# Optimization experiments

Hardware: AMD Instinct MI355X
Metric: run time of the kernel (lower is better)

The kernel has to match this reference:

```python
import jax, jax.numpy as jnp
import numpy as np

B, T, E, H = 64, 512, 256, 128


def setup_inputs() -> dict:
    key = jax.random.key(0)
    ks = jax.random.split(key, 7)
    s = 1.0 / np.sqrt(H)  # PyTorch LSTM default init range
    inputs = jax.random.normal(ks[0], (B, T, E), jnp.float32)
    labels = jax.random.randint(ks[1], (B, T), 0, H)
    W_ih = jax.random.uniform(ks[2], (4 * H, E), jnp.float32, -s, s)
    W_hh = jax.random.uniform(ks[3], (4 * H, H), jnp.float32, -s, s)
    b_ih = jax.random.uniform(ks[4], (4 * H,), jnp.float32, -s, s)
    b_hh = jax.random.uniform(ks[5], (4 * H,), jnp.float32, -s, s)
    transition = jax.random.uniform(ks[6], (H, H), jnp.float32)  # torch.rand
    return {"inputs": inputs, "labels": labels, "W_ih": W_ih, "W_hh": W_hh,
            "b_ih": b_ih, "b_hh": b_hh, "transition": transition}


def _lstm(x, W_ih, W_hh, b_ih, b_hh):
    # x: (T, B, E) -> hs: (T, B, H). PyTorch gate order: i, f, g, o.
    Bn = x.shape[1]
    Hn = W_hh.shape[1]

    def step(carry, xt):
        h, c = carry
        g = xt @ W_ih.T + b_ih + h @ W_hh.T + b_hh  # (B, 4H)
        i, f, gg, o = jnp.split(g, 4, axis=-1)
        c = jax.nn.sigmoid(f) * c + jax.nn.sigmoid(i) * jnp.tanh(gg)
        h = jax.nn.sigmoid(o) * jnp.tanh(c)
        return (h, c), h

    h0 = jnp.zeros((Bn, Hn), x.dtype)
    (_, _), hs = jax.lax.scan(step, (h0, h0), x)
    return hs


def reference(inputs, labels, W_ih, W_hh, b_ih, b_hh, transition):
    x = inputs.transpose(1, 0, 2)  # (T, B, E)
    trans = jax.nn.softmax(transition, axis=1)  # row-softmax transition
    hs = _lstm(x, W_ih, W_hh, b_ih, b_hh)  # (T, B, H)
    Hbth = jax.nn.softmax(hs, axis=2).transpose(1, 0, 2)  # (B, T, H)

    # gold-path score Pr: emissions at gold tags + transition scores
    emit = jnp.take_along_axis(Hbth, labels[:, :, None], axis=2)[..., 0].sum(axis=1)  # (B,)
    tr_score = trans[labels[:, :-1], labels[:, 1:]].sum(axis=1)  # (B,)
    Pr = emit + tr_score

    # CRF forward algorithm (partition score Ps) via scan over time
    pre0 = Hbth[:, 0, :] + trans[0]  # (B, H)

    def crf_step(pre, h_t):
        # Z[b, i, j] = pre[b, i] + trans[i, j] + h_t[b, j]
        Z = pre[:, :, None] + trans[None] + h_t[:, None, :]
        return jax.nn.logsumexp(Z, axis=1), None

    pre, _ = jax.lax.scan(crf_step, pre0, Hbth[:, 1:, :].transpose(1, 0, 2))
    Ps = jax.nn.logsumexp(pre + trans[-1][None, :], axis=1)  # (B,)

    return (Ps - Pr).sum()
```

## Files before the change

kernel.cpp:

```cpp
#include <hip/hip_runtime.h>
#include <hip/hip_bf16.h>
#include <cstdint>

#define BB 64
#define TT 512
#define EE 256
#define HH 128
#define G4 512

typedef _Float16 half2_t __attribute__((ext_vector_type(2)));
typedef _Float16 f16x4 __attribute__((ext_vector_type(4)));
typedef _Float16 f16x8 __attribute__((ext_vector_type(8)));
typedef float f32x4 __attribute__((ext_vector_type(4)));

#define BC(x) __builtin_bit_cast(half2_t, x)

#define BAR() asm volatile("s_waitcnt lgkmcnt(0)\n\ts_barrier" ::: "memory")

__device__ __forceinline__ float fdot2f(half2_t a, half2_t b, float c) {
#if defined(__has_builtin)
#if __has_builtin(__builtin_amdgcn_fdot2)
  return __builtin_amdgcn_fdot2(a, b, c, false);
#else
  return c + (float)a[0] * (float)b[0] + (float)a[1] * (float)b[1];
#endif
#else
  return c + (float)a[0] * (float)b[0] + (float)a[1] * (float)b[1];
#endif
}

__device__ __forceinline__ float rcp_(float x) { return __builtin_amdgcn_rcpf(x); }
__device__ __forceinline__ float tanh_(float x) {
  float ax = fabsf(x);
  float e = __expf(-2.f * ax);
  float r = (1.f - e) * rcp_(1.f + e);
  return copysignf(r, x);
}

__device__ __forceinline__ float readlane_f(float x, int lane) {
#if defined(__has_builtin)
#if __has_builtin(__builtin_amdgcn_readlane)
  return __builtin_bit_cast(float, __builtin_amdgcn_readlane(__builtin_bit_cast(int, x), lane));
#else
  return __shfl(x, lane);
#endif
#else
  return __shfl(x, lane);
#endif
}

#if defined(__has_builtin)
#if __has_builtin(__builtin_amdgcn_update_dpp)
#define HAVE_DPP 1
#endif
#endif

#ifdef HAVE_DPP
#define DPP_SHL(dst, src, N)                                                   \
  dst = __builtin_bit_cast(float, __builtin_amdgcn_update_dpp(                 \
            0, __builtin_bit_cast(int, src), 0x100 | (N), 0xf, 0xf, true))
#define DPP_QSWAP(dst, src)                                                    \
  dst = __builtin_bit_cast(float, __builtin_amdgcn_update_dpp(                 \
            0, __builtin_bit_cast(int, src), 0xB1, 0xf, 0xf, true))
#else
#define DPP_SHL(dst, src, N) dst = __shfl((src), (threadIdx.x & 63) + (N))
#define DPP_QSWAP(dst, src) dst = __shfl_xor((src), 1)
#endif

__device__ __forceinline__ float wave_sum64_bcast(float x) {
#ifdef HAVE_DPP
#define DPP_ADD(ctrl)                                                          \
  {                                                                            \
    int _t = __builtin_amdgcn_update_dpp(0, __builtin_bit_cast(int, x), ctrl,  \
                                         0xf, 0xf, true);                      \
    x += __builtin_bit_cast(float, _t);                                        \
  }
  DPP_ADD(0x111)
  DPP_ADD(0x112)
  DPP_ADD(0x114)
  DPP_ADD(0x118)
  DPP_ADD(0x142)
  DPP_ADD(0x143)
#undef DPP_ADD
  return readlane_f(x, 63);
#else
#pragma unroll
  for (int s = 1; s <= 32; s <<= 1) x += __shfl_xor(x, s);
  return x;
#endif
}

__device__ __host__ __forceinline__ int permj(int j) {
  return ((j & 127) << 2) | (j >> 7);
}

__global__ __launch_bounds__(128) void prep_kernel(
    const float* __restrict__ transition, const float* __restrict__ W_ih,
    float* __restrict__ trans, _Float16* __restrict__ W16) {
  const int bid = blockIdx.x, t = threadIdx.x;
  if (bid < 128) {
    __shared__ float red[2];
    float v = transition[bid * HH + t];
    float m = v;
#pragma unroll
    for (int s = 32; s >= 1; s >>= 1) m = fmaxf(m, __shfl_xor(m, s));
    if ((t & 63) == 0) red[t >> 6] = m;
    __syncthreads();
    m = fmaxf(red[0], red[1]);
    float e = __expf(v - m);
    float s = e;
#pragma unroll
    for (int k = 32; k >= 1; k >>= 1) s += __shfl_xor(s, k);
    __syncthreads();
    if ((t & 63) == 0) red[t >> 6] = s;
    __syncthreads();
    trans[bid * HH + t] = e * rcp_(red[0] + red[1]);
  } else {
    const int base = (bid - 128) * 1024 + t * 8;
    const int row = base >> 8;
    const int col = base & 255;
    float4 v0 = *(const float4*)(W_ih + base);
    float4 v1 = *(const float4*)(W_ih + base + 4);
    f16x8 h;
    h[0] = (_Float16)v0.x; h[1] = (_Float16)v0.y;
    h[2] = (_Float16)v0.z; h[3] = (_Float16)v0.w;
    h[4] = (_Float16)v1.x; h[5] = (_Float16)v1.y;
    h[6] = (_Float16)v1.z; h[7] = (_Float16)v1.w;
    *(f16x8*)(W16 + (size_t)permj(row) * EE + col) = h;
  }
}

__global__ __launch_bounds__(256) void gemm_in(
    const float* __restrict__ A, const _Float16* __restrict__ W16,
    const float* __restrict__ b_ih, const float* __restrict__ b_hh,
    float* __restrict__ out) {
  __shared__ _Float16 As[64][264];
  const int t = threadIdx.x;
  const int m0 = blockIdx.x * 64;
  const int n0 = blockIdx.y * 256;
  {
    const int c4 = t & 63, r0 = t >> 6;
#pragma unroll
    for (int p = 0; p < 16; ++p) {
      const int row = r0 + 4 * p;
      float4 v = *(const float4*)(A + (size_t)(m0 + row) * EE + c4 * 4);
      f16x4 h;
      h[0] = (_Float16)v.x; h[1] = (_Float16)v.y;
      h[2] = (_Float16)v.z; h[3] = (_Float16)v.w;
      *(f16x4*)&As[row][c4 * 4] = h;
    }
  }
  __syncthreads();
  const int w = t >> 6, L = t & 63;
  const int lrow = L & 15, quad = L >> 4, lk = quad * 8;
  f32x4 acc[4][4] = {};
  const _Float16* Wbase = W16 + (size_t)(n0 + w * 64) * EE;
#pragma unroll
  for (int kc = 0; kc < 8; ++kc) {
    f16x8 a[4], bf[4];
#pragma unroll
    for (int mf = 0; mf < 4; ++mf)
      a[mf] = *(const f16x8*)&As[mf * 16 + lrow][kc * 32 + lk];
#pragma unroll
    for (int nf = 0; nf < 4; ++nf)
      bf[nf] = *(const f16x8*)(Wbase + (size_t)(nf * 16 + lrow) * EE + kc * 32 + lk);
#pragma unroll
    for (int mf = 0; mf < 4; ++mf)
#pragma unroll
      for (int nf = 0; nf < 4; ++nf)
        acc[mf][nf] = __builtin_amdgcn_mfma_f32_16x16x32_f16(a[mf], bf[nf], acc[mf][nf], 0, 0, 0);
  }
#pragma unroll
  for (int nf = 0; nf < 4; ++nf) {
    const int j = n0 + w * 64 + nf * 16 + lrow;
    const int jo = ((j & 3) << 7) | (j >> 2);
    const float bias = b_ih[jo] + b_hh[jo];
#pragma unroll
    for (int mf = 0; mf < 4; ++mf) {
#pragma unroll
      for (int r = 0; r < 4; ++r) {
        const int m = m0 + mf * 16 + quad * 4 + r;
        out[(size_t)m * G4 + j] = acc[mf][nf][r] + bias;
      }
    }
  }
}

__global__ __launch_bounds__(768, 1)
__attribute__((amdgpu_waves_per_eu(3, 3)))
void lstm_crf(
    const float* __restrict__ precomp, const float* __restrict__ Whh,
    const float* __restrict__ trans, const int* __restrict__ labels,
    float* __restrict__ out_b) {
  const int b = blockIdx.x, t = threadIdx.x;
  const int w = t >> 6, l = t & 63, q = l >> 4, l15 = l & 15;
  const int tf_a = l15 & 3;
  const int gg = l15 >> 2;
  const bool isL = (w < 8);
  const int cl = t - 512;
  const int cw = cl >> 6;
  const int lcl = cl & 63;
  const int j = cl >> 1;
  const int kh = cl & 1;

  __shared__ __align__(16) _Float16 h16[4][HH];
  __shared__ __align__(16) float h32[4][HH];
  __shared__ __align__(16) _Float16 E16[2][HH];
  __shared__ float Mld[2][4];
  __shared__ float fin[12];
  __shared__ int lab[TT];

  f16x8 wfr[4][4];
  f32x4 pc_cur[4], pc_nxt[4];
  const float* pcb = nullptr;
  float c = 0.f;
  half2_t et[32];
  float tr0 = 0.f, tr127 = 0.f, pre = 0.f, emit = 0.f;

  if (isL) {
#pragma unroll
    for (int tf = 0; tf < 4; ++tf) {
      const int rowp = 16 * (4 * w + tf) + l15;
      const int u = rowp >> 2, g = rowp & 3;
      const float* src = Whh + (size_t)(g * HH + u) * HH;
#pragma unroll
      for (int kt = 0; kt < 4; ++kt) {
        const float* s8 = src + kt * 32 + q * 8;
        float4 v0 = *(const float4*)s8;
        float4 v1 = *(const float4*)(s8 + 4);
        f16x8 h8;
        h8[0] = (_Float16)v0.x; h8[1] = (_Float16)v0.y;
        h8[2] = (_Float16)v0.z; h8[3] = (_Float16)v0.w;
        h8[4] = (_Float16)v1.x; h8[5] = (_Float16)v1.y;
        h8[6] = (_Float16)v1.z; h8[7] = (_Float16)v1.w;
        wfr[tf][kt] = h8;
      }
    }
    pcb = precomp + (size_t)b * TT * G4 + 64 * w + 4 * q;
#pragma unroll
    for (int tf = 0; tf < 4; ++tf) pc_cur[tf] = *(const f32x4*)(pcb + 16 * tf);
  } else {
#pragma unroll
    for (int a = 0; a < 32; ++a) {
      const int i0 = 64 * kh + 2 * a;
      float e0 = __expf(trans[i0 * HH + j]);
      float e1 = __expf(trans[(i0 + 1) * HH + j]);
      half2_t h2; h2[0] = (_Float16)e0; h2[1] = (_Float16)e1;
      et[a] = h2;
    }
    tr0 = trans[j];
    tr127 = trans[127 * HH + j];
  }
  if (t < TT) lab[t] = labels[b * TT + t];
  if (t < HH) { h16[0][t] = (_Float16)0.f; h32[0][t] = 0.f; }
  __syncthreads();

#pragma unroll 1
  for (int s = 0; s <= TT; ++s) {
    if (isL) {
      if (s < TT) {
        const int sn = (s < TT - 1) ? s + 1 : s;
#pragma unroll
        for (int tf = 0; tf < 4; ++tf)
          pc_nxt[tf] = *(const f32x4*)(pcb + (size_t)sn * G4 + 16 * tf);
        const int rs = s & 3;
        const f16x8 hb0 = *(const f16x8*)&h16[rs][q * 8];
        const f16x8 hb1 = *(const f16x8*)&h16[rs][32 + q * 8];
        const f16x8 hb2 = *(const f16x8*)&h16[rs][64 + q * 8];
        const f16x8 hb3 = *(const f16x8*)&h16[rs][96 + q * 8];
        f32x4 a0 = pc_cur[0], a1 = pc_cur[1], a2 = pc_cur[2], a3 = pc_cur[3];
        a0 = __builtin_amdgcn_mfma_f32_16x16x32_f16(wfr[0][0], hb0, a0, 0, 0, 0);
        a1 = __builtin_amdgcn_mfma_f32_16x16x32_f16(wfr[1][0], hb0, a1, 0, 0, 0);
        a2 = __builtin_amdgcn_mfma_f32_16x16x32_f16(wfr[2][0], hb0, a2, 0, 0, 0);
        a3 = __builtin_amdgcn_mfma_f32_16x16x32_f16(wfr[3][0], hb0, a3, 0, 0, 0);
        a0 = __builtin_amdgcn_mfma_f32_16x16x32_f16(wfr[0][1], hb1, a0, 0, 0, 0);
        a1 = __builtin_amdgcn_mfma_f32_16x16x32_f16(wfr[1][1], hb1, a1, 0, 0, 0);
        a2 = __builtin_amdgcn_mfma_f32_16x16x32_f16(wfr[2][1], hb1, a2, 0, 0, 0);
        a3 = __builtin_amdgcn_mfma_f32_16x16x32_f16(wfr[3][1], hb1, a3, 0, 0, 0);
        a0 = __builtin_amdgcn_mfma_f32_16x16x32_f16(wfr[0][2], hb2, a0, 0, 0, 0);
        a1 = __builtin_amdgcn_mfma_f32_16x16x32_f16(wfr[1][2], hb2, a1, 0, 0, 0);
        a2 = __builtin_amdgcn_mfma_f32_16x16x32_f16(wfr[2][2], hb2, a2, 0, 0, 0);
        a3 = __builtin_amdgcn_mfma_f32_16x16x32_f16(wfr[3][2], hb2, a3, 0, 0, 0);
        a0 = __builtin_amdgcn_mfma_f32_16x16x32_f16(wfr[0][3], hb3, a0, 0, 0, 0);
        a1 = __builtin_amdgcn_mfma_f32_16x16x32_f16(wfr[1][3], hb3, a1, 0, 0, 0);
        a2 = __builtin_amdgcn_mfma_f32_16x16x32_f16(wfr[2][3], hb3, a2, 0, 0, 0);
        a3 = __builtin_amdgcn_mfma_f32_16x16x32_f16(wfr[3][3], hb3, a3, 0, 0, 0);
        const f32x4 asel = (tf_a == 0) ? a0 : (tf_a == 1) ? a1 : (tf_a == 2) ? a2 : a3;
        const float gv = (gg == 0) ? asel[0] : (gg == 1) ? asel[1]
                       : (gg == 2) ? asel[2] : asel[3];
        const bool isg = (gg == 2);
        const float yy = isg ? (-2.f * fabsf(gv)) : (-gv);
        const float exv = __expf(yy);
        const float num = isg ? (1.f - exv) : 1.f;
        float av = num * rcp_(1.f + exv);
        av = isg ? copysignf(av, gv) : av;
        float Fv, Gv, Ov;
        DPP_SHL(Fv, av, 4);
        DPP_SHL(Gv, av, 8);
        DPP_SHL(Ov, av, 12);
        c = Fv * c + av * Gv;
        const float hv = Ov * tanh_(c);
        if (gg == 0) {
          const int ua = 16 * w + 4 * l15 + q;
          h16[(s + 1) & 3][ua] = (_Float16)hv;
          h32[(s + 1) & 3][ua] = hv;
        }
#pragma unroll
        for (int tf = 0; tf < 4; ++tf) pc_cur[tf] = pc_nxt[tf];
      }
    } else if (s >= 1) {
      const int rs = s & 3;
      const float2 hp = *(const float2*)&h32[rs][2 * lcl];
      const float denom = wave_sum64_bcast(__expf(hp.x) + __expf(hp.y));
      const float hj = h32[rs][j];
      const float p = __expf(hj) * rcp_(denom);
      if (s == 1) {
        pre = p + tr0;
      } else {
        const int rp = (s & 1) ^ 1;
        float Sa = 0.f, Sb = 0.f;
        const float4* ev = (const float4*)&E16[rp][64 * kh];
#pragma unroll
        for (int ec = 0; ec < 4; ++ec) {
          const float4 eb = ev[ec];
          Sa = fdot2f(et[4 * ec + 0], BC(eb.x), Sa);
          Sa = fdot2f(et[4 * ec + 1], BC(eb.y), Sa);
          Sa = fdot2f(et[4 * ec + 2], BC(eb.z), Sa);
          Sa = fdot2f(et[4 * ec + 3], BC(eb.w), Sa);
        }
#pragma unroll
        for (int ec = 4; ec < 8; ++ec) {
          const float4 eb = ev[ec];
          Sb = fdot2f(et[4 * ec + 0], BC(eb.x), Sb);
          Sb = fdot2f(et[4 * ec + 1], BC(eb.y), Sb);
          Sb = fdot2f(et[4 * ec + 2], BC(eb.z), Sb);
          Sb = fdot2f(et[4 * ec + 3], BC(eb.w), Sb);
        }
        const float M0 = Mld[rp][0], M1 = Mld[rp][1];
        const float M2 = Mld[rp][2], M3 = Mld[rp][3];
        const float Cc = fmaxf(fmaxf(M0, M1), fmaxf(M2, M3));
        const float Ma = (kh == 0) ? M0 : M2;
        const float Mb = (kh == 0) ? M1 : M3;
        float Sp = __expf(Ma - Cc) * Sa + __expf(Mb - Cc) * Sb;
        float Spo;
        DPP_QSWAP(Spo, Sp);
        pre = p + Cc + __logf(Sp + Spo);
      }
      if (kh == 0 && j == lab[s - 1]) emit += p;
      const float Mw = readlane_f(pre, 0);
      if (kh == 0) E16[s & 1][j] = (_Float16)__expf(pre - Mw);
      if (lcl == 0) Mld[s & 1][cw] = Mw;
    }
    BAR();
  }
  if (!isL) {
    float v = (kh == 0) ? (pre + tr127) : -3.0e38f;
#pragma unroll
    for (int s2 = 1; s2 <= 32; s2 <<= 1) v = fmaxf(v, __shfl_xor(v, s2));
    if (lcl == 0) fin[cw] = v;
  }
  __syncthreads();
  if (!isL) {
    const float C4 = fmaxf(fmaxf(fin[0], fin[1]), fmaxf(fin[2], fin[3]));
    float ex = (kh == 0) ? __expf(pre + tr127 - C4) : 0.f;
    float em = emit;
#pragma unroll
    for (int s2 = 1; s2 <= 32; s2 <<= 1) {
      ex += __shfl_xor(ex, s2);
      em += __shfl_xor(em, s2);
    }
    if (lcl == 0) { fin[4 + cw] = ex; fin[8 + cw] = em; }
  }
  __syncthreads();
  if (t == 0) {
    const float C4 = fmaxf(fmaxf(fin[0], fin[1]), fmaxf(fin[2], fin[3]));
    out_b[b] = C4 + __logf(fin[4] + fin[5] + fin[6] + fin[7]) -
               (fin[8] + fin[9] + fin[10] + fin[11]);
  }
}

__global__ __launch_bounds__(512) void finalize_kernel(
    const float* __restrict__ trans, const int* __restrict__ labels,
    const float* __restrict__ out_b, float* __restrict__ d_out) {
  const int t = threadIdx.x;
  float a = 0.f;
  if (t < TT - 1) {
    for (int b = 0; b < BB; ++b) {
      const int l0 = labels[b * TT + t];
      const int l1 = labels[b * TT + t + 1];
      a += trans[l0 * HH + l1];
    }
  }
  float x = ((t < BB) ? out_b[t] : 0.f) - a;
  __shared__ float red[8];
#pragma unroll
  for (int s = 32; s >= 1; s >>= 1) x += __shfl_xor(x, s);
  if ((t & 63) == 0) red[t >> 6] = x;
  __syncthreads();
  if (t == 0) {
    float s = 0.f;
#pragma unroll
    for (int i = 0; i < 8; ++i) s += red[i];
    d_out[0] = s;
  }
}

extern "C" void kernel_launch(void* const* d_in, const int* in_sizes, int n_in,
                              void* d_out, int out_size, void* d_ws, size_t ws_size,
                              hipStream_t stream) {
  const float* inputs = (const float*)d_in[0];
  const int* labels = (const int*)d_in[1];
  const float* W_ih = (const float*)d_in[2];
  const float* W_hh = (const float*)d_in[3];
  const float* b_ih = (const float*)d_in[4];
  const float* b_hh = (const float*)d_in[5];
  const float* transition = (const float*)d_in[6];

  char* ws = (char*)d_ws;
  float* precomp = (float*)ws;
  float* trans = (float*)(ws + 67108864);
  _Float16* W16 = (_Float16*)(ws + 67108864 + 65536);
  float* out_b = (float*)(ws + 67108864 + 65536 + 262144);

  prep_kernel<<<256, 128, 0, stream>>>(transition, W_ih, trans, W16);
  gemm_in<<<dim3(512, 2), 256, 0, stream>>>(inputs, W16, b_ih, b_hh, precomp);
  lstm_crf<<<64, 768, 0, stream>>>(precomp, W_hh, trans, labels, out_b);
  finalize_kernel<<<1, 512, 0, stream>>>(trans, labels, out_b, (float*)d_out);
}
```

Before: 511.1 us.

## Unroll recurrence by two with ping-pong buffers and two-step precomp prefetch

Unrolls the fused LSTM/CRF time loop by two using a PHASE macro with compile-time buffer indices. The 4-deep h buffers shrink to 2 and the CRF steps get fixed parities. Precomputed gate inputs are now prefetched two steps ahead into alternating register sets, removing the per-step register copy and hiding more global latency. The MFMA chain is wrapped in s_setprio, Mld is read as one float4, and the last CRF step is peeled out of the loop. The risk is that two h buffers with one barrier per step may be too few for safe reuse.

```diff
diff --git a/kernel.cpp b/kernel.cpp
--- a/kernel.cpp
+++ b/kernel.cpp
@@ -203,16 +203,16 @@
   const int j = cl >> 1;
   const int kh = cl & 1;
 
-  __shared__ __align__(16) _Float16 h16[4][HH];
-  __shared__ __align__(16) float h32[4][HH];
+  __shared__ __align__(16) _Float16 h16[2][HH];
+  __shared__ __align__(16) float h32[2][HH];
   __shared__ __align__(16) _Float16 E16[2][HH];
-  __shared__ float Mld[2][4];
+  __shared__ __align__(16) float Mld[2][4];
   __shared__ float fin[12];
   __shared__ int lab[TT];
 
   f16x8 wfr[4][4];
-  f32x4 pc_cur[4], pc_nxt[4];
-  const float* pcb = nullptr;
+  f32x4 pcA[4], pcB[4];
+  const float* pnext = nullptr;
   float c = 0.f;
   half2_t et[32];
   float tr0 = 0.f, tr127 = 0.f, pre = 0.f, emit = 0.f;
@@ -236,9 +236,13 @@
         wfr[tf][kt] = h8;
       }
     }
-    pcb = precomp + (size_t)b * TT * G4 + 64 * w + 4 * q;
-#pragma unroll
-    for (int tf = 0; tf < 4; ++tf) pc_cur[tf] = *(const f32x4*)(pcb + 16 * tf);
+    const float* pcb = precomp + (size_t)b * TT * G4 + 64 * w + 4 * q;
+#pragma unroll
+    for (int tf = 0; tf < 4; ++tf) {
+      pcA[tf] = *(const f32x4*)(pcb + 16 * tf);
+      pcB[tf] = *(const f32x4*)(pcb + G4 + 16 * tf);
+    }
+    pnext = pcb + 2 * G4;
   } else {
 #pragma unroll
     for (int a = 0; a < 32; ++a) {
@@ -255,103 +259,147 @@
   if (t < HH) { h16[0][t] = (_Float16)0.f; h32[0][t] = 0.f; }
   __syncthreads();
 
+#define PHASE(PR, SS, PCV, PREFETCH)                                           \
+  if (isL) {                                                                   \
+    const f16x8 hb0 = *(const f16x8*)&h16[PR][q * 8];                          \
+    const f16x8 hb1 = *(const f16x8*)&h16[PR][32 + q * 8];                     \
+    const f16x8 hb2 = *(const f16x8*)&h16[PR][64 + q * 8];                     \
+    const f16x8 hb3 = *(const f16x8*)&h16[PR][96 + q * 8];                     \
+    f32x4 a0 = PCV[0], a1 = PCV[1], a2 = PCV[2], a3 = PCV[3];                  \
+    PREFETCH                                                                   \
+    __builtin_amdgcn_s_setprio(1);                                             \
+    a0 = __builtin_amdgcn_mfma_f32_16x16x32_f16(wfr[0][0], hb0, a0, 0, 0, 0);  \
+    a1 = __builtin_amdgcn_mfma_f32_16x16x32_f16(wfr[1][0], hb0, a1, 0, 0, 0);  \
+    a2 = __builtin_amdgcn_mfma_f32_16x16x32_f16(wfr[2][0], hb0, a2, 0, 0, 0);  \
+    a3 = __builtin_amdgcn_mfma_f32_16x16x32_f16(wfr[3][0], hb0, a3, 0, 0, 0);  \
+    a0 = __builtin_amdgcn_mfma_f32_16x16x32_f16(wfr[0][1], hb1, a0, 0, 0, 0);  \
+    a1 = __builtin_amdgcn_mfma_f32_16x16x32_f16(wfr[1][1], hb1, a1, 0, 0, 0);  \
+    a2 = __builtin_amdgcn_mfma_f32_16x16x32_f16(wfr[2][1], hb1, a2, 0, 0, 0);  \
+    a3 = __builtin_amdgcn_mfma_f32_16x16x32_f16(wfr[3][1], hb1, a3, 0, 0, 0);  \
+    a0 = __builtin_amdgcn_mfma_f32_16x16x32_f16(wfr[0][2], hb2, a0, 0, 0, 0);  \
+    a1 = __builtin_amdgcn_mfma_f32_16x16x32_f16(wfr[1][2], hb2, a1, 0, 0, 0);  \
+    a2 = __builtin_amdgcn_mfma_f32_16x16x32_f16(wfr[2][2], hb2, a2, 0, 0, 0);  \
+    a3 = __builtin_amdgcn_mfma_f32_16x16x32_f16(wfr[3][2], hb2, a3, 0, 0, 0);  \
+    a0 = __builtin_amdgcn_mfma_f32_16x16x32_f16(wfr[0][3], hb3, a0, 0, 0, 0);  \
+    a1 = __builtin_amdgcn_mfma_f32_16x16x32_f16(wfr[1][3], hb3, a1, 0, 0, 0);  \
+    a2 = __builtin_amdgcn_mfma_f32_16x16x32_f16(wfr[2][3], hb3, a2, 0, 0, 0);  \
+    a3 = __builtin_amdgcn_mfma_f32_16x16x32_f16(wfr[3][3], hb3, a3, 0, 0, 0);  \
+    __builtin_amdgcn_s_setprio(0);                                             \
+    const f32x4 asel = (tf_a == 0) ? a0 : (tf_a == 1) ? a1                     \
+                     : (tf_a == 2) ? a2 : a3;                                  \
+    const float gv = (gg == 0) ? asel[0] : (gg == 1) ? asel[1]                 \
+                   : (gg == 2) ? asel[2] : asel[3];                            \
+    const bool isg = (gg == 2);                                                \
+    const float yy = isg ? (-2.f * fabsf(gv)) : (-gv);                         \
+    const float exv = __expf(yy);                                              \
+    const float num = isg ? (1.f - exv) : 1.f;                                 \
+    float av = num * rcp_(1.f + exv);                                          \
+    av = isg ? copysignf(av, gv) : av;                                         \
+    float Fv, Gv, Ov;                                                          \
+    DPP_SHL(Fv, av, 4);                                                        \
+    DPP_SHL(Gv, av, 8);                                                        \
+    DPP_SHL(Ov, av, 12);                                                       \
+    c = Fv * c + av * Gv;                                                      \
+    const float hv = Ov * tanh_(c);                                            \
+    if (gg == 0) {                                                             \
+      const int ua = 16 * w + 4 * l15 + q;                                     \
+      h16[(PR) ^ 1][ua] = (_Float16)hv;                                        \
+      h32[(PR) ^ 1][ua] = hv;                                                  \
+    }                                                                          \
+  } else if ((SS) >= 1) {                                                      \
+    const float2 hp = *(const float2*)&h32[PR][2 * lcl];                       \
+    const float denom = wave_sum64_bcast(__expf(hp.x) + __expf(hp.y));         \
+    const float hj = h32[PR][j];                                               \
+    const float p = __expf(hj) * rcp_(denom);                                  \
+    if ((SS) == 1) {                                                           \
+      pre = p + tr0;                                                           \
+    } else {                                                                   \
+      float Sa = 0.f, Sb = 0.f;                                                \
+      const float4* ev = (const float4*)&E16[(PR) ^ 1][64 * kh];               \
+      _Pragma("unroll")                                                        \
+      for (int ec = 0; ec < 4; ++ec) {                                         \
+        const float4 eb = ev[ec];                                              \
+        Sa = fdot2f(et[4 * ec + 0], BC(eb.x), Sa);                             \
+        Sa = fdot2f(et[4 * ec + 1], BC(eb.y), Sa);                             \
+        Sa = fdot2f(et[4 * ec + 2], BC(eb.z), Sa);                             \
+        Sa = fdot2f(et[4 * ec + 3], BC(eb.w), Sa);                             \
+      }                                                                        \
+      _Pragma("unroll")                                                        \
+      for (int ec = 4; ec < 8; ++ec) {                                         \
+        const float4 eb = ev[ec];                                              \
+        Sb = fdot2f(et[4 * ec + 0], BC(eb.x), Sb);                             \
+        Sb = fdot2f(et[4 * ec + 1], BC(eb.y), Sb);                             \
+        Sb = fdot2f(et[4 * ec + 2], BC(eb.z), Sb);                             \
+        Sb = fdot2f(et[4 * ec + 3], BC(eb.w), Sb);                             \
+      }                                                                        \
+      const float4 Mv = *(const float4*)&Mld[(PR) ^ 1][0];                     \
+      const float Cc = fmaxf(fmaxf(Mv.x, Mv.y), fmaxf(Mv.z, Mv.w));            \
+      const float Ma = (kh == 0) ? Mv.x : Mv.z;                                \
+      const float Mb = (kh == 0) ? Mv.y : Mv.w;                                \
+      float Sp = __expf(Ma - Cc) * Sa + __expf(Mb - Cc) * Sb;                  \
+      float Spo;                                                               \
+      DPP_QSWAP(Spo, Sp);                                                      \
+      pre = p + Cc + __logf(Sp + Spo);                                         \
+    }                                                                          \
+    if (kh == 0 && j == lab[(SS) - 1]) emit += p;                              \
+    const float Mw = readlane_f(pre, 0);                                       \
+    if (kh == 0) E16[PR][j] = (_Float16)__expf(pre - Mw);                      \
+    if (lcl == 0) Mld[PR][cw] = Mw;                                            \
+  }                                                                            \
+  BAR();
+
 #pragma unroll 1
-  for (int s = 0; s <= TT; ++s) {
-    if (isL) {
-      if (s < TT) {
-        const int sn = (s < TT - 1) ? s + 1 : s;
-#pragma unroll
-        for (int tf = 0; tf < 4; ++tf)
-          pc_nxt[tf] = *(const f32x4*)(pcb + (size_t)sn * G4 + 16 * tf);
-        const int rs = s & 3;
-        const f16x8 hb0 = *(const f16x8*)&h16[rs][q * 8];
-        const f16x8 hb1 = *(const f16x8*)&h16[rs][32 + q * 8];
-        const f16x8 hb2 = *(const f16x8*)&h16[rs][64 + q * 8];
-        const f16x8 hb3 = *(const f16x8*)&h16[rs][96 + q * 8];
-        f32x4 a0 = pc_cur[0], a1 = pc_cur[1], a2 = pc_cur[2], a3 = pc_cur[3];
-        a0 = __builtin_amdgcn_mfma_f32_16x16x32_f16(wfr[0][0], hb0, a0, 0, 0, 0);
-        a1 = __builtin_amdgcn_mfma_f32_16x16x32_f16(wfr[1][0], hb0, a1, 0, 0, 0);
-        a2 = __builtin_amdgcn_mfma_f32_16x16x32_f16(wfr[2][0], hb0, a2, 0, 0, 0);
-        a3 = __builtin_amdgcn_mfma_f32_16x16x32_f16(wfr[3][0], hb0, a3, 0, 0, 0);
-        a0 = __builtin_amdgcn_mfma_f32_16x16x32_f16(wfr[0][1], hb1, a0, 0, 0, 0);
-        a1 = __builtin_amdgcn_mfma_f32_16x16x32_f16(wfr[1][1], hb1, a1, 0, 0, 0);
-        a2 = __builtin_amdgcn_mfma_f32_16x16x32_f16(wfr[2][1], hb1, a2, 0, 0, 0);
-        a3 = __builtin_amdgcn_mfma_f32_16x16x32_f16(wfr[3][1], hb1, a3, 0, 0, 0);
-        a0 = __builtin_amdgcn_mfma_f32_16x16x32_f16(wfr[0][2], hb2, a0, 0, 0, 0);
-        a1 = __builtin_amdgcn_mfma_f32_16x16x32_f16(wfr[1][2], hb2, a1, 0, 0, 0);
-        a2 = __builtin_amdgcn_mfma_f32_16x16x32_f16(wfr[2][2], hb2, a2, 0, 0, 0);
-        a3 = __builtin_amdgcn_mfma_f32_16x16x32_f16(wfr[3][2], hb2, a3, 0, 0, 0);
-        a0 = __builtin_amdgcn_mfma_f32_16x16x32_f16(wfr[0][3], hb3, a0, 0, 0, 0);
-        a1 = __builtin_amdgcn_mfma_f32_16x16x32_f16(wfr[1][3], hb3, a1, 0, 0, 0);
-        a2 = __builtin_amdgcn_mfma_f32_16x16x32_f16(wfr[2][3], hb3, a2, 0, 0, 0);
-        a3 = __builtin_amdgcn_mfma_f32_16x16x32_f16(wfr[3][3], hb3, a3, 0, 0, 0);
-        const f32x4 asel = (tf_a == 0) ? a0 : (tf_a == 1) ? a1 : (tf_a == 2) ? a2 : a3;
-        const float gv = (gg == 0) ? asel[0] : (gg == 1) ? asel[1]
-                       : (gg == 2) ? asel[2] : asel[3];
-        const bool isg = (gg == 2);
-        const float yy = isg ? (-2.f * fabsf(gv)) : (-gv);
-        const float exv = __expf(yy);
-        const float num = isg ? (1.f - exv) : 1.f;
-        float av = num * rcp_(1.f + exv);
-        av = isg ? copysignf(av, gv) : av;
-        float Fv, Gv, Ov;
-        DPP_SHL(Fv, av, 4);
-        DPP_SHL(Gv, av, 8);
-        DPP_SHL(Ov, av, 12);
-        c = Fv * c + av * Gv;
-        const float hv = Ov * tanh_(c);
-        if (gg == 0) {
-          const int ua = 16 * w + 4 * l15 + q;
-          h16[(s + 1) & 3][ua] = (_Float16)hv;
-          h32[(s + 1) & 3][ua] = hv;
-        }
-#pragma unroll
-        for (int tf = 0; tf < 4; ++tf) pc_cur[tf] = pc_nxt[tf];
+  for (int k = 0; k < 256; ++k) {
+    PHASE(0, 2 * k, pcA,
+          if (k < 255) {
+            pcA[0] = *(const f32x4*)(pnext);
+            pcA[1] = *(const f32x4*)(pnext + 16);
+            pcA[2] = *(const f32x4*)(pnext + 32);
+            pcA[3] = *(const f32x4*)(pnext + 48);
+          })
+    PHASE(1, 2 * k + 1, pcB,
+          if (k < 255) {
+            pcB[0] = *(const f32x4*)(pnext + G4);
+            pcB[1] = *(const f32x4*)(pnext + G4 + 16);
+            pcB[2] = *(const f32x4*)(pnext + G4 + 32);
+            pcB[3] = *(const f32x4*)(pnext + G4 + 48);
+          })
+    pnext += 2 * G4;
+  }
+  if (!isL) {
+    const float2 hp = *(const float2*)&h32[0][2 * lcl];
+    const float denom = wave_sum64_bcast(__expf(hp.x) + __expf(hp.y));
+    const float hj = h32[0][j];
+    const float p = __expf(hj) * rcp_(denom);
+    {
+      float Sa = 0.f, Sb = 0.f;
+      const float4* ev = (const float4*)&E16[1][64 * kh];
+#pragma unroll
+      for (int ec = 0; ec < 4; ++ec) {
+        const float4 eb = ev[ec];
+        Sa = fdot2f(et[4 * ec + 0], BC(eb.x), Sa);
+        Sa = fdot2f(et[4 * ec + 1], BC(eb.y), Sa);
+        Sa = fdot2f(et[4 * ec + 2], BC(eb.z), Sa);
+        Sa = fdot2f(et[4 * ec + 3], BC(eb.w), Sa);
       }
-    } else if (s >= 1) {
-      const int rs = s & 3;
-      const float2 hp = *(const float2*)&h32[rs][2 * lcl];
-      const float denom = wave_sum64_bcast(__expf(hp.x) + __expf(hp.y));
-      const float hj = h32[rs][j];
-      const float p = __expf(hj) * rcp_(denom);
-      if (s == 1) {
-        pre = p + tr0;
-      } else {
-        const int rp = (s & 1) ^ 1;
-        float Sa = 0.f, Sb = 0.f;
-        const float4* ev = (const float4*)&E16[rp][64 * kh];
-#pragma unroll
-        for (int ec = 0; ec < 4; ++ec) {
-          const float4 eb = ev[ec];
-          Sa = fdot2f(et[4 * ec + 0], BC(eb.x), Sa);
-          Sa = fdot2f(et[4 * ec + 1], BC(eb.y), Sa);
-          Sa = fdot2f(et[4 * ec + 2], BC(eb.z), Sa);
-          Sa = fdot2f(et[4 * ec + 3], BC(eb.w), Sa);
-        }
-#pragma unroll
-        for (int ec = 4; ec < 8; ++ec) {
-          const float4 eb = ev[ec];
-          Sb = fdot2f(et[4 * ec + 0], BC(eb.x), Sb);
-          Sb = fdot2f(et[4 * ec + 1], BC(eb.y), Sb);
-          Sb = fdot2f(et[4 * ec + 2], BC(eb.z), Sb);
-          Sb = fdot2f(et[4 * ec + 3], BC(eb.w), Sb);
-        }
-        const float M0 = Mld[rp][0], M1 = Mld[rp][1];
-        const float M2 = Mld[rp][2], M3 = Mld[rp][3];
-        const float Cc = fmaxf(fmaxf(M0, M1), fmaxf(M2, M3));
-        const float Ma = (kh == 0) ? M0 : M2;
-        const float Mb = (kh == 0) ? M1 : M3;
-        float Sp = __expf(Ma - Cc) * Sa + __expf(Mb - Cc) * Sb;
-        float Spo;
-        DPP_QSWAP(Spo, Sp);
-        pre = p + Cc + __logf(Sp + Spo);
+#pragma unroll
+      for (int ec = 4; ec < 8; ++ec) {
+        const float4 eb = ev[ec];
+        Sb = fdot2f(et[4 * ec + 0], BC(eb.x), Sb);
+        Sb = fdot2f(et[4 * ec + 1], BC(eb.y), Sb);
+        Sb = fdot2f(et[4 * ec + 2], BC(eb.z), Sb);
+        Sb = fdot2f(et[4 * ec + 3], BC(eb.w), Sb);
       }
-      if (kh == 0 && j == lab[s - 1]) emit += p;
-      const float Mw = readlane_f(pre, 0);
-      if (kh == 0) E16[s & 1][j] = (_Float16)__expf(pre - Mw);
-      if (lcl == 0) Mld[s & 1][cw] = Mw;
-    }
-    BAR();
+      const float4 Mv = *(const float4*)&Mld[1][0];
+      const float Cc = fmaxf(fmaxf(Mv.x, Mv.y), fmaxf(Mv.z, Mv.w));
+      const float Ma = (kh == 0) ? Mv.x : Mv.z;
+      const float Mb = (kh == 0) ? Mv.y : Mv.w;
+      float Sp = __expf(Ma - Cc) * Sa + __expf(Mb - Cc) * Sb;
+      float Spo;
+      DPP_QSWAP(Spo, Sp);
+      pre = p + Cc + __logf(Sp + Spo);
+    }
+    if (kh == 0 && j == lab[TT - 1]) emit += p;
   }
   if (!isL) {
     float v = (kh == 0) ? (pre + tr127) : -3.0e38f;
```

Result: slower. 768.7 us (+50.4%).
